# Kernel tuning notes

Measured on AMD Instinct MI355X. Metric: run time of the kernel, lower is better.

The kernel has to match this reference:

```python
import jax, jax.numpy as jnp
import numpy as np

EMBED_DIM = 1024
NUM_HEADS = 16
DEPTH = EMBED_DIM // NUM_HEADS  # 64
B, S = 4, 2048


def setup_inputs() -> dict:
    key = jax.random.key(0)
    ks = jax.random.split(key, 12)
    sc = 0.02
    return {
        "q": jax.random.normal(ks[0], (B, S, EMBED_DIM), jnp.float32),
        "k": jax.random.normal(ks[1], (B, S, EMBED_DIM), jnp.float32),
        "v": jax.random.normal(ks[2], (B, S, EMBED_DIM), jnp.float32),
        # per-head Dense(depth) weights stacked over heads: [H, D, depth]
        "wq": jax.random.normal(ks[3], (NUM_HEADS, EMBED_DIM, DEPTH), jnp.float32) * sc,
        "bq": jnp.zeros((NUM_HEADS, DEPTH), jnp.float32),
        "wk": jax.random.normal(ks[4], (NUM_HEADS, EMBED_DIM, DEPTH), jnp.float32) * sc,
        "bk": jnp.zeros((NUM_HEADS, DEPTH), jnp.float32),
        "wv": jax.random.normal(ks[5], (NUM_HEADS, EMBED_DIM, DEPTH), jnp.float32) * sc,
        "bv": jnp.zeros((NUM_HEADS, DEPTH), jnp.float32),
        # final Dense(embedding_dim): [D, D]
        "wo": jax.random.normal(ks[6], (EMBED_DIM, EMBED_DIM), jnp.float32) * sc,
        "bo": jnp.zeros((EMBED_DIM,), jnp.float32),
        "use_mask": 1,
    }


def reference(q, k, v, wq, bq, wk, bk, wv, bv, wo, bo, use_mask):
    # Batched per-head projections (equivalent to H separate Dense layers).
    qh = jnp.einsum('bsd,hde->bhse', q, wq) + bq[None, :, None, :]
    kh = jnp.einsum('bsd,hde->bhse', k, wk) + bk[None, :, None, :]
    vh = jnp.einsum('bsd,hde->bhse', v, wv) + bv[None, :, None, :]

    scale = 1.0 / jnp.sqrt(jnp.asarray(DEPTH, jnp.float32))
    logits = jnp.einsum('bhqe,bhke->bhqk', qh, kh) * scale  # [B,H,Sq,Sk]
    if use_mask:
        Sq, Sk = qh.shape[2], kh.shape[2]
        causal = jnp.triu(jnp.ones((Sq, Sk), jnp.float32), k=1)
        logits = logits + causal[None, None, :, :] * (-1e9)
    attn = jax.nn.softmax(logits, axis=-1)
    out_h = jnp.einsum('bhqk,bhke->bhqe', attn, vh)  # [B,H,Sq,depth]
    # concat heads along last dim -> [B,Sq,H*depth]
    bsz, H, Sq, dep = out_h.shape
    concat = out_h.transpose(0, 2, 1, 3).reshape(bsz, Sq, H * dep)
    return concat @ wo + bo
```

## Files before the change

### kernel.cpp

```cpp
#include <hip/hip_runtime.h>

#define B_ 4
#define S_ 2048
#define H_ 16
#define D_ 64
#define E_ 1024
#define M_ 8192

typedef __attribute__((ext_vector_type(8))) __bf16 bf16x8;
typedef __attribute__((ext_vector_type(4))) __bf16 bf16x4;
typedef __attribute__((ext_vector_type(4))) float f32x4;
typedef __attribute__((ext_vector_type(16))) float f32x16;

__device__ __forceinline__ void gload_lds16(const void* g, void* l) {
  __builtin_amdgcn_global_load_lds(
      (const __attribute__((address_space(1))) unsigned int*)g,
      (__attribute__((address_space(3))) unsigned int*)l, 16, 0, 0);
}

__device__ __forceinline__ unsigned pk2(float a, float b) {
  union { __bf16 h; unsigned short u; } ua, ub;
  ua.h = (__bf16)a; ub.h = (__bf16)b;
  return ((unsigned)ub.u << 16) | (unsigned)ua.u;
}

__global__ void cvt_all(const float* __restrict__ q, const float* __restrict__ k,
                        const float* __restrict__ v, __bf16* __restrict__ Aq,
                        __bf16* __restrict__ Ak, __bf16* __restrict__ Av) {
  const int y = blockIdx.y;
  const float* src = (y == 0) ? q : (y == 1) ? k : v;
  __bf16* dst = (y == 0) ? Aq : (y == 1) ? Ak : Av;
  const int i = blockIdx.x * blockDim.x + threadIdx.x;
  const float4 vv = ((const float4*)src)[i];
  bf16x4 o;
  o.x = (__bf16)vv.x; o.y = (__bf16)vv.y; o.z = (__bf16)vv.z; o.w = (__bf16)vv.w;
  ((bf16x4*)dst)[i] = o;
}

__global__ void pack_all(const float* __restrict__ wq, const float* __restrict__ wk,
                         const float* __restrict__ wv, const float* __restrict__ wo,
                         __bf16* __restrict__ Bq, __bf16* __restrict__ Bk,
                         __bf16* __restrict__ Bv, __bf16* __restrict__ Bo) {
  const int y = blockIdx.y;
  const int idx = blockIdx.x * 256 + threadIdx.x;
  const int n = idx >> 10, kk = idx & 1023;
  if (y < 3) {
    const float* w = (y == 0) ? wq : (y == 1) ? wk : wv;
    __bf16* out = (y == 0) ? Bq : (y == 1) ? Bk : Bv;
    out[idx] = (__bf16)w[((size_t)(n >> 6) << 16) + (kk << 6) + (n & 63)];
  } else {
    Bo[idx] = (__bf16)wo[((size_t)kk << 10) + n];
  }
}

template <int MODE>
__global__ __launch_bounds__(256) void gemm_bt(const __bf16* __restrict__ A,
                                               const __bf16* __restrict__ Bt,
                                               const float* __restrict__ bias,
                                               void* __restrict__ Cout) {
  constexpr int K = 1024;
  __shared__ __bf16 As[128 * 64];
  __shared__ __bf16 Bs[128 * 64];
  const int t = threadIdx.x;
  const int w = t >> 6, l = t & 63;
  const int m0 = blockIdx.x * 128, n0 = blockIdx.y * 128;
  f32x4 acc[4][4] = {};

  for (int kt = 0; kt < K / 64; ++kt) {
    const int kb = kt * 64;
#pragma unroll
    for (int j = 0; j < 4; ++j) {
      const int ci = (j * 4 + w) * 64 + l;
      const int row = ci >> 3;
      const int c = (ci & 7) ^ (row & 7);
      gload_lds16(A + (size_t)(m0 + row) * K + kb + c * 8, As + (j * 4 + w) * 512);
      gload_lds16(Bt + (size_t)(n0 + row) * K + kb + c * 8, Bs + (j * 4 + w) * 512);
    }
    __syncthreads();
#pragma unroll
    for (int kk = 0; kk < 64; kk += 32) {
      bf16x8 af[4], bfr[4];
#pragma unroll
      for (int f = 0; f < 4; ++f) {
        const int ra = (w >> 1) * 64 + f * 16 + (l & 15);
        const int ca = ((kk >> 3) + (l >> 4)) ^ (ra & 7);
        af[f] = *(const bf16x8*)(As + ra * 64 + ca * 8);
        const int rb = (w & 1) * 64 + f * 16 + (l & 15);
        const int cb = ((kk >> 3) + (l >> 4)) ^ (rb & 7);
        bfr[f] = *(const bf16x8*)(Bs + rb * 64 + cb * 8);
      }
#pragma unroll
      for (int mf = 0; mf < 4; ++mf)
#pragma unroll
        for (int nf = 0; nf < 4; ++nf)
          acc[mf][nf] = __builtin_amdgcn_mfma_f32_16x16x32_bf16(af[mf], bfr[nf],
                                                                acc[mf][nf], 0, 0, 0);
    }
    __syncthreads();
  }

#pragma unroll
  for (int mf = 0; mf < 4; ++mf) {
#pragma unroll
    for (int nf = 0; nf < 4; ++nf) {
#pragma unroll
      for (int r = 0; r < 4; ++r) {
        const int gm = m0 + (w >> 1) * 64 + mf * 16 + (l >> 4) * 4 + r;
        const int gn = n0 + (w & 1) * 64 + nf * 16 + (l & 15);
        const float val = acc[mf][nf][r] + ((MODE == 1) ? bias[gm] : bias[gn]);
        if constexpr (MODE == 0) {
          ((__bf16*)Cout)[(((size_t)(gm >> 11) * H_ + (gn >> 6)) * S_ + (gm & 2047)) * D_ + (gn & 63)] =
              (__bf16)val;
        } else if constexpr (MODE == 1) {
          ((__bf16*)Cout)[(((size_t)(gn >> 11) * H_ + (gm >> 6)) * D_ + (gm & 63)) * S_ + (gn & 2047)] =
              (__bf16)val;
        } else {
          ((float*)Cout)[(size_t)gm * 1024 + gn] = val;
        }
      }
    }
  }
}

__global__ __launch_bounds__(512, 2) void attn_fused(const __bf16* __restrict__ qh,
                                                     const __bf16* __restrict__ kh,
                                                     const __bf16* __restrict__ vT,
                                                     __bf16* __restrict__ concat,
                                                     const int* __restrict__ use_mask_p) {
  __shared__ __bf16 Ks[2][64 * 64];
  __shared__ __bf16 Vs[2][64 * 64];
  const int t = threadIdx.x, w = t >> 6, l = t & 63;
  const int lo = l & 31, hi = l >> 5;
  const int bh = blockIdx.x, pair = blockIdx.y;
  const int usemask = *use_mask_p;
  const __bf16* Qb = qh + (size_t)bh * S_ * D_;
  const __bf16* Kb = kh + (size_t)bh * S_ * D_;
  const __bf16* Vb = vT + (size_t)bh * D_ * S_;
  const int b = bh >> 4, hh = bh & 15;
  constexpr float CEXP = 0.125f * 1.4426950408889634f;

  const int srow = t >> 3;
  const int sc = (t & 7) ^ (srow & 7);

  int cur = 0;
  for (int half = 0; half < 2; ++half) {
    const int qt = half ? (7 - pair) : pair;
    const int qrow0 = qt * 256 + w * 32;
    const int nkt = usemask ? (4 * qt + 4) : (S_ / 64);
    const int ktw = usemask ? (4 * qt + (w >> 1)) : 100000;
    const int ktdiag = usemask ? (4 * qt + (w >> 1)) : -1;

    bf16x8 qf[4];
#pragma unroll
    for (int ks = 0; ks < 4; ++ks)
      qf[ks] = *(const bf16x8*)(Qb + (size_t)(qrow0 + lo) * D_ + ks * 16 + hi * 8);

    float m = -3e38f, ls = 0.f;
    f32x16 o0 = {}, o1 = {};

    gload_lds16(Kb + (size_t)(0 + srow) * D_ + sc * 8, &Ks[cur][w * 512]);
    gload_lds16(Vb + (size_t)srow * S_ + 0 + sc * 8, &Vs[cur][w * 512]);

    for (int kt = 0; kt < nkt; ++kt) {
      __builtin_amdgcn_sched_barrier(0);
      asm volatile("s_waitcnt vmcnt(0)" ::: "memory");
      __builtin_amdgcn_s_barrier();
      __builtin_amdgcn_sched_barrier(0);

      if (kt + 1 < nkt) {
        const int nxt = cur ^ 1;
        gload_lds16(Kb + (size_t)((kt + 1) * 64 + srow) * D_ + sc * 8, &Ks[nxt][w * 512]);
        gload_lds16(Vb + (size_t)srow * S_ + (kt + 1) * 64 + sc * 8, &Vs[nxt][w * 512]);
      }

      if (kt <= ktw) {
        f32x16 s0 = {}, s1 = {};
        __builtin_amdgcn_s_setprio(1);
#pragma unroll
        for (int ks = 0; ks < 4; ++ks) {
          const int ch = ((ks << 1) | hi) ^ (lo & 7);
          const bf16x8 k0 = *(const bf16x8*)(&Ks[cur][lo * 64 + ch * 8]);
          const bf16x8 k1 = *(const bf16x8*)(&Ks[cur][(32 + lo) * 64 + ch * 8]);
          s0 = __builtin_amdgcn_mfma_f32_32x32x16_bf16(k0, qf[ks], s0, 0, 0, 0);
          s1 = __builtin_amdgcn_mfma_f32_32x32x16_bf16(k1, qf[ks], s1, 0, 0, 0);
        }
        __builtin_amdgcn_s_setprio(0);

        if (kt == ktdiag) {
          const int qloc = ((w & 1) << 5) + lo;
#pragma unroll
          for (int r = 0; r < 16; ++r) {
            const int kv0 = (r & 3) + 8 * (r >> 2) + 4 * hi;
            if (kv0 > qloc) s0[r] = -1e30f;
            if (kv0 + 32 > qloc) s1[r] = -1e30f;
          }
        }

        float pm = s0[0];
#pragma unroll
        for (int r = 1; r < 16; ++r) pm = fmaxf(pm, s0[r]);
#pragma unroll
        for (int r = 0; r < 16; ++r) pm = fmaxf(pm, s1[r]);
        pm = fmaxf(pm, __shfl_xor(pm, 32));

        if (!__all(pm - m <= 64.0f)) {
          const float mn = fmaxf(m, pm);
          const float al = __builtin_amdgcn_exp2f((m - mn) * CEXP);
          m = mn;
          ls *= al;
          o0 *= al;
          o1 *= al;
        }

        unsigned W0[4][2], W1[4][2];
        float rs0 = 0.f, rs1 = 0.f;
#pragma unroll
        for (int j = 0; j < 4; ++j) {
          float p0 = __builtin_amdgcn_exp2f((s0[4 * j + 0] - m) * CEXP);
          float p1 = __builtin_amdgcn_exp2f((s0[4 * j + 1] - m) * CEXP);
          float p2 = __builtin_amdgcn_exp2f((s0[4 * j + 2] - m) * CEXP);
          float p3 = __builtin_amdgcn_exp2f((s0[4 * j + 3] - m) * CEXP);
          rs0 += (p0 + p1) + (p2 + p3);
          W0[j][0] = pk2(p0, p1);
          W0[j][1] = pk2(p2, p3);
          float q0 = __builtin_amdgcn_exp2f((s1[4 * j + 0] - m) * CEXP);
          float q1 = __builtin_amdgcn_exp2f((s1[4 * j + 1] - m) * CEXP);
          float q2 = __builtin_amdgcn_exp2f((s1[4 * j + 2] - m) * CEXP);
          float q3 = __builtin_amdgcn_exp2f((s1[4 * j + 3] - m) * CEXP);
          rs1 += (q0 + q1) + (q2 + q3);
          W1[j][0] = pk2(q0, q1);
          W1[j][1] = pk2(q2, q3);
        }
        float rs = rs0 + rs1;
        rs += __shfl_xor(rs, 32);
        ls += rs;

        bf16x8 pa[4];
#pragma unroll
        for (int ks = 0; ks < 4; ++ks) {
          const int c = ks & 1;
          unsigned x0, x1, y0, y1;
          if ((ks >> 1) == 0) {
            x0 = W0[2 * c][0]; x1 = W0[2 * c][1];
            y0 = W0[2 * c + 1][0]; y1 = W0[2 * c + 1][1];
          } else {
            x0 = W1[2 * c][0]; x1 = W1[2 * c][1];
            y0 = W1[2 * c + 1][0]; y1 = W1[2 * c + 1][1];
          }
          asm volatile("v_permlane32_swap_b32 %0, %1" : "+v"(x0), "+v"(y0));
          asm volatile("v_permlane32_swap_b32 %0, %1" : "+v"(x1), "+v"(y1));
          union { unsigned u[4]; bf16x8 v; } uu;
          uu.u[0] = x0; uu.u[1] = x1; uu.u[2] = y0; uu.u[3] = y1;
          pa[ks] = uu.v;
        }

        __builtin_amdgcn_s_setprio(1);
#pragma unroll
        for (int ks = 0; ks < 4; ++ks) {
          const int ch = ((ks << 1) | hi) ^ (lo & 7);
          const bf16x8 v0 = *(const bf16x8*)(&Vs[cur][lo * 64 + ch * 8]);
          const bf16x8 v1 = *(const bf16x8*)(&Vs[cur][(32 + lo) * 64 + ch * 8]);
          o0 = __builtin_amdgcn_mfma_f32_32x32x16_bf16(v0, pa[ks], o0, 0, 0, 0);
          o1 = __builtin_amdgcn_mfma_f32_32x32x16_bf16(v1, pa[ks], o1, 0, 0, 0);
        }
        __builtin_amdgcn_s_setprio(0);
      }
      cur ^= 1;
    }

    const float inv = 1.0f / ls;
    const size_t rowbase = ((size_t)(b * S_ + qrow0 + lo)) * E_ + hh * 64;
#pragma unroll
    for (int rr = 0; rr < 4; ++rr) {
      bf16x4 v0, v1;
#pragma unroll
      for (int bb = 0; bb < 4; ++bb) {
        v0[bb] = (__bf16)(o0[4 * rr + bb] * inv);
        v1[bb] = (__bf16)(o1[4 * rr + bb] * inv);
      }
      *(bf16x4*)(concat + rowbase + 8 * rr + 4 * hi) = v0;
      *(bf16x4*)(concat + rowbase + 32 + 8 * rr + 4 * hi) = v1;
    }
  }
}

extern "C" void kernel_launch(void* const* d_in, const int* in_sizes, int n_in,
                              void* d_out, int out_size, void* d_ws, size_t ws_size,
                              hipStream_t stream) {
  const float* q = (const float*)d_in[0];
  const float* k = (const float*)d_in[1];
  const float* v = (const float*)d_in[2];
  const float* wq = (const float*)d_in[3];
  const float* bq = (const float*)d_in[4];
  const float* wk = (const float*)d_in[5];
  const float* bk = (const float*)d_in[6];
  const float* wv = (const float*)d_in[7];
  const float* bv = (const float*)d_in[8];
  const float* wo = (const float*)d_in[9];
  const float* bo = (const float*)d_in[10];
  const int* use_mask = (const int*)d_in[11];
  (void)in_sizes; (void)n_in; (void)out_size; (void)ws_size;

  char* ws = (char*)d_ws;
  __bf16* Aq = (__bf16*)ws;
  __bf16* Ak = Aq + (size_t)M_ * E_;
  __bf16* Av = Ak + (size_t)M_ * E_;
  __bf16* Bq = Av + (size_t)M_ * E_;
  __bf16* Bk = Bq + (size_t)E_ * E_;
  __bf16* Bv = Bk + (size_t)E_ * E_;
  __bf16* Bo = Bv + (size_t)E_ * E_;
  __bf16* qhb = Bo + (size_t)E_ * E_;
  __bf16* khb = qhb + (size_t)8388608;
  __bf16* vTb = khb + (size_t)8388608;
  __bf16* concat = Aq;

  cvt_all<<<dim3(8192, 3), 256, 0, stream>>>(q, k, v, Aq, Ak, Av);
  pack_all<<<dim3(4096, 4), 256, 0, stream>>>(wq, wk, wv, wo, Bq, Bk, Bv, Bo);
  gemm_bt<0><<<dim3(64, 8), 256, 0, stream>>>(Aq, Bq, bq, qhb);
  gemm_bt<0><<<dim3(64, 8), 256, 0, stream>>>(Ak, Bk, bk, khb);
  gemm_bt<1><<<dim3(8, 64), 256, 0, stream>>>(Bv, Av, bv, vTb);
  attn_fused<<<dim3(64, 4), 512, 0, stream>>>(qhb, khb, vTb, concat, use_mask);
  gemm_bt<2><<<dim3(64, 8), 256, 0, stream>>>(concat, Bo, bo, d_out);
}
```

Measured before the change: 207.0 us.

## Give each attention wave 64 query rows and one q-tile per block

The attention kernel moves from 8 waves of 32 query rows to 4 waves of 64 query rows each, so every K/V fragment read from LDS feeds twice as many MFMAs. Each block now handles a single 256-row query tile, with 8 tiles in the y-grid ordered heaviest first, instead of pairing two tiles per block for load balance. The goal is less LDS read traffic per unit of work and more instruction-level parallelism per wave. The cost is higher register pressure from the doubled accumulators and Q fragments, and per-block work that is now uneven under the causal mask.

```diff
diff --git a/kernel.cpp b/kernel.cpp
--- a/kernel.cpp
+++ b/kernel.cpp
@@ -122,7 +122,7 @@
   }
 }
 
-__global__ __launch_bounds__(512, 2) void attn_fused(const __bf16* __restrict__ qh,
+__global__ __launch_bounds__(256, 2) void attn_fused(const __bf16* __restrict__ qh,
                                                      const __bf16* __restrict__ kh,
                                                      const __bf16* __restrict__ vT,
                                                      __bf16* __restrict__ concat,
@@ -131,7 +131,9 @@
   __shared__ __bf16 Vs[2][64 * 64];
   const int t = threadIdx.x, w = t >> 6, l = t & 63;
   const int lo = l & 31, hi = l >> 5;
-  const int bh = blockIdx.x, pair = blockIdx.y;
+  const int bh = blockIdx.x;
+  const int y = blockIdx.y;
+  const int qt = (y < 4) ? (7 - y) : (y - 4);
   const int usemask = *use_mask_p;
   const __bf16* Qb = qh + (size_t)bh * S_ * D_;
   const __bf16* Kb = kh + (size_t)bh * S_ * D_;
@@ -139,147 +141,196 @@
   const int b = bh >> 4, hh = bh & 15;
   constexpr float CEXP = 0.125f * 1.4426950408889634f;
 
-  const int srow = t >> 3;
-  const int sc = (t & 7) ^ (srow & 7);
+  const int qrow0 = qt * 256 + w * 64;
+  const int nkt = usemask ? (4 * qt + 4) : (S_ / 64);
+  const int ktw = usemask ? (4 * qt + w) : (1 << 30);
+
+  bf16x8 qfA[4], qfB[4];
+#pragma unroll
+  for (int ks = 0; ks < 4; ++ks) {
+    qfA[ks] = *(const bf16x8*)(Qb + (size_t)(qrow0 + lo) * D_ + ks * 16 + hi * 8);
+    qfB[ks] = *(const bf16x8*)(Qb + (size_t)(qrow0 + 32 + lo) * D_ + ks * 16 + hi * 8);
+  }
+
+  float mA = -3e38f, mB = -3e38f, lsA = 0.f, lsB = 0.f;
+  f32x16 oA0 = {}, oA1 = {}, oB0 = {}, oB1 = {};
 
   int cur = 0;
-  for (int half = 0; half < 2; ++half) {
-    const int qt = half ? (7 - pair) : pair;
-    const int qrow0 = qt * 256 + w * 32;
-    const int nkt = usemask ? (4 * qt + 4) : (S_ / 64);
-    const int ktw = usemask ? (4 * qt + (w >> 1)) : 100000;
-    const int ktdiag = usemask ? (4 * qt + (w >> 1)) : -1;
-
-    bf16x8 qf[4];
-#pragma unroll
-    for (int ks = 0; ks < 4; ++ks)
-      qf[ks] = *(const bf16x8*)(Qb + (size_t)(qrow0 + lo) * D_ + ks * 16 + hi * 8);
-
-    float m = -3e38f, ls = 0.f;
-    f32x16 o0 = {}, o1 = {};
-
-    gload_lds16(Kb + (size_t)(0 + srow) * D_ + sc * 8, &Ks[cur][w * 512]);
-    gload_lds16(Vb + (size_t)srow * S_ + 0 + sc * 8, &Vs[cur][w * 512]);
-
-    for (int kt = 0; kt < nkt; ++kt) {
-      __builtin_amdgcn_sched_barrier(0);
-      asm volatile("s_waitcnt vmcnt(0)" ::: "memory");
-      __builtin_amdgcn_s_barrier();
-      __builtin_amdgcn_sched_barrier(0);
-
-      if (kt + 1 < nkt) {
-        const int nxt = cur ^ 1;
-        gload_lds16(Kb + (size_t)((kt + 1) * 64 + srow) * D_ + sc * 8, &Ks[nxt][w * 512]);
-        gload_lds16(Vb + (size_t)srow * S_ + (kt + 1) * 64 + sc * 8, &Vs[nxt][w * 512]);
-      }
-
-      if (kt <= ktw) {
-        f32x16 s0 = {}, s1 = {};
-        __builtin_amdgcn_s_setprio(1);
-#pragma unroll
-        for (int ks = 0; ks < 4; ++ks) {
-          const int ch = ((ks << 1) | hi) ^ (lo & 7);
-          const bf16x8 k0 = *(const bf16x8*)(&Ks[cur][lo * 64 + ch * 8]);
-          const bf16x8 k1 = *(const bf16x8*)(&Ks[cur][(32 + lo) * 64 + ch * 8]);
-          s0 = __builtin_amdgcn_mfma_f32_32x32x16_bf16(k0, qf[ks], s0, 0, 0, 0);
-          s1 = __builtin_amdgcn_mfma_f32_32x32x16_bf16(k1, qf[ks], s1, 0, 0, 0);
-        }
-        __builtin_amdgcn_s_setprio(0);
-
-        if (kt == ktdiag) {
-          const int qloc = ((w & 1) << 5) + lo;
-#pragma unroll
-          for (int r = 0; r < 16; ++r) {
-            const int kv0 = (r & 3) + 8 * (r >> 2) + 4 * hi;
-            if (kv0 > qloc) s0[r] = -1e30f;
-            if (kv0 + 32 > qloc) s1[r] = -1e30f;
-          }
-        }
-
-        float pm = s0[0];
-#pragma unroll
-        for (int r = 1; r < 16; ++r) pm = fmaxf(pm, s0[r]);
-#pragma unroll
-        for (int r = 0; r < 16; ++r) pm = fmaxf(pm, s1[r]);
-        pm = fmaxf(pm, __shfl_xor(pm, 32));
-
-        if (!__all(pm - m <= 64.0f)) {
-          const float mn = fmaxf(m, pm);
-          const float al = __builtin_amdgcn_exp2f((m - mn) * CEXP);
-          m = mn;
-          ls *= al;
-          o0 *= al;
-          o1 *= al;
-        }
-
+  {
+#pragma unroll
+    for (int j = 0; j < 2; ++j) {
+      const int ci = j * 256 + t;
+      const int row = ci >> 3;
+      const int sc = (ci & 7) ^ (row & 7);
+      gload_lds16(Kb + (size_t)row * D_ + sc * 8, &Ks[0][j * 2048 + w * 512]);
+      gload_lds16(Vb + (size_t)row * S_ + sc * 8, &Vs[0][j * 2048 + w * 512]);
+    }
+  }
+
+  for (int kt = 0; kt < nkt; ++kt) {
+    __builtin_amdgcn_sched_barrier(0);
+    asm volatile("s_waitcnt vmcnt(0)" ::: "memory");
+    __builtin_amdgcn_s_barrier();
+    __builtin_amdgcn_sched_barrier(0);
+
+    if (kt + 1 < nkt) {
+      const int nxt = cur ^ 1;
+#pragma unroll
+      for (int j = 0; j < 2; ++j) {
+        const int ci = j * 256 + t;
+        const int row = ci >> 3;
+        const int sc = (ci & 7) ^ (row & 7);
+        gload_lds16(Kb + (size_t)((kt + 1) * 64 + row) * D_ + sc * 8,
+                    &Ks[nxt][j * 2048 + w * 512]);
+        gload_lds16(Vb + (size_t)row * S_ + (kt + 1) * 64 + sc * 8,
+                    &Vs[nxt][j * 2048 + w * 512]);
+      }
+    }
+
+    if (kt <= ktw) {
+      f32x16 sA0 = {}, sA1 = {}, sB0 = {}, sB1 = {};
+      __builtin_amdgcn_s_setprio(1);
+#pragma unroll
+      for (int ks = 0; ks < 4; ++ks) {
+        const int ch = ((ks << 1) | hi) ^ (lo & 7);
+        const bf16x8 k0 = *(const bf16x8*)(&Ks[cur][lo * 64 + ch * 8]);
+        const bf16x8 k1 = *(const bf16x8*)(&Ks[cur][(32 + lo) * 64 + ch * 8]);
+        sA0 = __builtin_amdgcn_mfma_f32_32x32x16_bf16(k0, qfA[ks], sA0, 0, 0, 0);
+        sA1 = __builtin_amdgcn_mfma_f32_32x32x16_bf16(k1, qfA[ks], sA1, 0, 0, 0);
+        sB0 = __builtin_amdgcn_mfma_f32_32x32x16_bf16(k0, qfB[ks], sB0, 0, 0, 0);
+        sB1 = __builtin_amdgcn_mfma_f32_32x32x16_bf16(k1, qfB[ks], sB1, 0, 0, 0);
+      }
+      __builtin_amdgcn_s_setprio(0);
+
+      if (usemask && kt == ktw) {
+#pragma unroll
+        for (int r = 0; r < 16; ++r) {
+          const int c = (r & 3) + 8 * (r >> 2) + 4 * hi;
+          if (c > lo) sA0[r] = -1e30f;
+          sA1[r] = -1e30f;
+          if (c > lo) sB1[r] = -1e30f;
+        }
+      }
+
+      float pmA = sA0[0], pmB = sB0[0];
+#pragma unroll
+      for (int r = 1; r < 16; ++r) { pmA = fmaxf(pmA, sA0[r]); pmB = fmaxf(pmB, sB0[r]); }
+#pragma unroll
+      for (int r = 0; r < 16; ++r) { pmA = fmaxf(pmA, sA1[r]); pmB = fmaxf(pmB, sB1[r]); }
+      pmA = fmaxf(pmA, __shfl_xor(pmA, 32));
+      pmB = fmaxf(pmB, __shfl_xor(pmB, 32));
+
+      if (!__all((pmA - mA <= 64.0f) && (pmB - mB <= 64.0f))) {
+        const float mnA = fmaxf(mA, pmA), mnB = fmaxf(mB, pmB);
+        const float alA = __builtin_amdgcn_exp2f((mA - mnA) * CEXP);
+        const float alB = __builtin_amdgcn_exp2f((mB - mnB) * CEXP);
+        mA = mnA; mB = mnB;
+        lsA *= alA; lsB *= alB;
+        oA0 *= alA; oA1 *= alA; oB0 *= alB; oB1 *= alB;
+      }
+
+      bf16x8 paA[4], paB[4];
+      {
         unsigned W0[4][2], W1[4][2];
-        float rs0 = 0.f, rs1 = 0.f;
+        float rs = 0.f;
 #pragma unroll
         for (int j = 0; j < 4; ++j) {
-          float p0 = __builtin_amdgcn_exp2f((s0[4 * j + 0] - m) * CEXP);
-          float p1 = __builtin_amdgcn_exp2f((s0[4 * j + 1] - m) * CEXP);
-          float p2 = __builtin_amdgcn_exp2f((s0[4 * j + 2] - m) * CEXP);
-          float p3 = __builtin_amdgcn_exp2f((s0[4 * j + 3] - m) * CEXP);
-          rs0 += (p0 + p1) + (p2 + p3);
-          W0[j][0] = pk2(p0, p1);
-          W0[j][1] = pk2(p2, p3);
-          float q0 = __builtin_amdgcn_exp2f((s1[4 * j + 0] - m) * CEXP);
-          float q1 = __builtin_amdgcn_exp2f((s1[4 * j + 1] - m) * CEXP);
-          float q2 = __builtin_amdgcn_exp2f((s1[4 * j + 2] - m) * CEXP);
-          float q3 = __builtin_amdgcn_exp2f((s1[4 * j + 3] - m) * CEXP);
-          rs1 += (q0 + q1) + (q2 + q3);
-          W1[j][0] = pk2(q0, q1);
-          W1[j][1] = pk2(q2, q3);
-        }
-        float rs = rs0 + rs1;
+          float p0 = __builtin_amdgcn_exp2f((sA0[4 * j + 0] - mA) * CEXP);
+          float p1 = __builtin_amdgcn_exp2f((sA0[4 * j + 1] - mA) * CEXP);
+          float p2 = __builtin_amdgcn_exp2f((sA0[4 * j + 2] - mA) * CEXP);
+          float p3 = __builtin_amdgcn_exp2f((sA0[4 * j + 3] - mA) * CEXP);
+          rs += (p0 + p1) + (p2 + p3);
+          W0[j][0] = pk2(p0, p1); W0[j][1] = pk2(p2, p3);
+          float q0 = __builtin_amdgcn_exp2f((sA1[4 * j + 0] - mA) * CEXP);
+          float q1 = __builtin_amdgcn_exp2f((sA1[4 * j + 1] - mA) * CEXP);
+          float q2 = __builtin_amdgcn_exp2f((sA1[4 * j + 2] - mA) * CEXP);
+          float q3 = __builtin_amdgcn_exp2f((sA1[4 * j + 3] - mA) * CEXP);
+          rs += (q0 + q1) + (q2 + q3);
+          W1[j][0] = pk2(q0, q1); W1[j][1] = pk2(q2, q3);
+        }
         rs += __shfl_xor(rs, 32);
-        ls += rs;
-
-        bf16x8 pa[4];
+        lsA += rs;
 #pragma unroll
         for (int ks = 0; ks < 4; ++ks) {
           const int c = ks & 1;
           unsigned x0, x1, y0, y1;
-          if ((ks >> 1) == 0) {
-            x0 = W0[2 * c][0]; x1 = W0[2 * c][1];
-            y0 = W0[2 * c + 1][0]; y1 = W0[2 * c + 1][1];
-          } else {
-            x0 = W1[2 * c][0]; x1 = W1[2 * c][1];
-            y0 = W1[2 * c + 1][0]; y1 = W1[2 * c + 1][1];
-          }
+          if ((ks >> 1) == 0) { x0 = W0[2 * c][0]; x1 = W0[2 * c][1]; y0 = W0[2 * c + 1][0]; y1 = W0[2 * c + 1][1]; }
+          else { x0 = W1[2 * c][0]; x1 = W1[2 * c][1]; y0 = W1[2 * c + 1][0]; y1 = W1[2 * c + 1][1]; }
           asm volatile("v_permlane32_swap_b32 %0, %1" : "+v"(x0), "+v"(y0));
           asm volatile("v_permlane32_swap_b32 %0, %1" : "+v"(x1), "+v"(y1));
           union { unsigned u[4]; bf16x8 v; } uu;
           uu.u[0] = x0; uu.u[1] = x1; uu.u[2] = y0; uu.u[3] = y1;
-          pa[ks] = uu.v;
-        }
-
-        __builtin_amdgcn_s_setprio(1);
+          paA[ks] = uu.v;
+        }
+      }
+      {
+        unsigned W0[4][2], W1[4][2];
+        float rs = 0.f;
+#pragma unroll
+        for (int j = 0; j < 4; ++j) {
+          float p0 = __builtin_amdgcn_exp2f((sB0[4 * j + 0] - mB) * CEXP);
+          float p1 = __builtin_amdgcn_exp2f((sB0[4 * j + 1] - mB) * CEXP);
+          float p2 = __builtin_amdgcn_exp2f((sB0[4 * j + 2] - mB) * CEXP);
+          float p3 = __builtin_amdgcn_exp2f((sB0[4 * j + 3] - mB) * CEXP);
+          rs += (p0 + p1) + (p2 + p3);
+          W0[j][0] = pk2(p0, p1); W0[j][1] = pk2(p2, p3);
+          float q0 = __builtin_amdgcn_exp2f((sB1[4 * j + 0] - mB) * CEXP);
+          float q1 = __builtin_amdgcn_exp2f((sB1[4 * j + 1] - mB) * CEXP);
+          float q2 = __builtin_amdgcn_exp2f((sB1[4 * j + 2] - mB) * CEXP);
+          float q3 = __builtin_amdgcn_exp2f((sB1[4 * j + 3] - mB) * CEXP);
+          rs += (q0 + q1) + (q2 + q3);
+          W1[j][0] = pk2(q0, q1); W1[j][1] = pk2(q2, q3);
+        }
+        rs += __shfl_xor(rs, 32);
+        lsB += rs;
 #pragma unroll
         for (int ks = 0; ks < 4; ++ks) {
-          const int ch = ((ks << 1) | hi) ^ (lo & 7);
-          const bf16x8 v0 = *(const bf16x8*)(&Vs[cur][lo * 64 + ch * 8]);
-          const bf16x8 v1 = *(const bf16x8*)(&Vs[cur][(32 + lo) * 64 + ch * 8]);
-          o0 = __builtin_amdgcn_mfma_f32_32x32x16_bf16(v0, pa[ks], o0, 0, 0, 0);
-          o1 = __builtin_amdgcn_mfma_f32_32x32x16_bf16(v1, pa[ks], o1, 0, 0, 0);
-        }
-        __builtin_amdgcn_s_setprio(0);
-      }
-      cur ^= 1;
-    }
-
-    const float inv = 1.0f / ls;
-    const size_t rowbase = ((size_t)(b * S_ + qrow0 + lo)) * E_ + hh * 64;
+          const int c = ks & 1;
+          unsigned x0, x1, y0, y1;
+          if ((ks >> 1) == 0) { x0 = W0[2 * c][0]; x1 = W0[2 * c][1]; y0 = W0[2 * c + 1][0]; y1 = W0[2 * c + 1][1]; }
+          else { x0 = W1[2 * c][0]; x1 = W1[2 * c][1]; y0 = W1[2 * c + 1][0]; y1 = W1[2 * c + 1][1]; }
+          asm volatile("v_permlane32_swap_b32 %0, %1" : "+v"(x0), "+v"(y0));
+          asm volatile("v_permlane32_swap_b32 %0, %1" : "+v"(x1), "+v"(y1));
+          union { unsigned u[4]; bf16x8 v; } uu;
+          uu.u[0] = x0; uu.u[1] = x1; uu.u[2] = y0; uu.u[3] = y1;
+          paB[ks] = uu.v;
+        }
+      }
+
+      __builtin_amdgcn_s_setprio(1);
+#pragma unroll
+      for (int ks = 0; ks < 4; ++ks) {
+        const int ch = ((ks << 1) | hi) ^ (lo & 7);
+        const bf16x8 v0 = *(const bf16x8*)(&Vs[cur][lo * 64 + ch * 8]);
+        const bf16x8 v1 = *(const bf16x8*)(&Vs[cur][(32 + lo) * 64 + ch * 8]);
+        oA0 = __builtin_amdgcn_mfma_f32_32x32x16_bf16(v0, paA[ks], oA0, 0, 0, 0);
+        oA1 = __builtin_amdgcn_mfma_f32_32x32x16_bf16(v1, paA[ks], oA1, 0, 0, 0);
+        oB0 = __builtin_amdgcn_mfma_f32_32x32x16_bf16(v0, paB[ks], oB0, 0, 0, 0);
+        oB1 = __builtin_amdgcn_mfma_f32_32x32x16_bf16(v1, paB[ks], oB1, 0, 0, 0);
+      }
+      __builtin_amdgcn_s_setprio(0);
+    }
+    cur ^= 1;
+  }
+
+  {
+    const float invA = 1.0f / lsA, invB = 1.0f / lsB;
+    const size_t rbA = ((size_t)(b * S_ + qrow0 + lo)) * E_ + hh * 64;
+    const size_t rbB = ((size_t)(b * S_ + qrow0 + 32 + lo)) * E_ + hh * 64;
 #pragma unroll
     for (int rr = 0; rr < 4; ++rr) {
-      bf16x4 v0, v1;
+      bf16x4 a0, a1, b0, b1;
 #pragma unroll
       for (int bb = 0; bb < 4; ++bb) {
-        v0[bb] = (__bf16)(o0[4 * rr + bb] * inv);
-        v1[bb] = (__bf16)(o1[4 * rr + bb] * inv);
-      }
-      *(bf16x4*)(concat + rowbase + 8 * rr + 4 * hi) = v0;
-      *(bf16x4*)(concat + rowbase + 32 + 8 * rr + 4 * hi) = v1;
+        a0[bb] = (__bf16)(oA0[4 * rr + bb] * invA);
+        a1[bb] = (__bf16)(oA1[4 * rr + bb] * invA);
+        b0[bb] = (__bf16)(oB0[4 * rr + bb] * invB);
+        b1[bb] = (__bf16)(oB1[4 * rr + bb] * invB);
+      }
+      *(bf16x4*)(concat + rbA + 8 * rr + 4 * hi) = a0;
+      *(bf16x4*)(concat + rbA + 32 + 8 * rr + 4 * hi) = a1;
+      *(bf16x4*)(concat + rbB + 8 * rr + 4 * hi) = b0;
+      *(bf16x4*)(concat + rbB + 32 + 8 * rr + 4 * hi) = b1;
     }
   }
 }
@@ -319,6 +370,6 @@
   gemm_bt<0><<<dim3(64, 8), 256, 0, stream>>>(Aq, Bq, bq, qhb);
   gemm_bt<0><<<dim3(64, 8), 256, 0, stream>>>(Ak, Bk, bk, khb);
   gemm_bt<1><<<dim3(8, 64), 256, 0, stream>>>(Bv, Av, bv, vTb);
-  attn_fused<<<dim3(64, 4), 512, 0, stream>>>(qhb, khb, vTb, concat, use_mask);
+  attn_fused<<<dim3(64, 8), 256, 0, stream>>>(qhb, khb, vTb, concat, use_mask);
   gemm_bt<2><<<dim3(64, 8), 256, 0, stream>>>(concat, Bo, bo, d_out);
 }
```

Result: no change. 210.5 us (+1.7%).

## Merge Q/K projection GEMMs and halve attention block size for more blocks

Applied to the files above, without the earlier changes.

Fuses the separate Q and K projection GEMM launches into one launch of 1024 blocks, so the GPU fills better and one launch is saved. The attention kernel moves from 512-thread blocks over 256-row query tiles to 256-thread blocks over 128-row tiles. That doubles the grid to 512 blocks, with K/V tile loads split across two passes per thread. The softmax exponent now uses one fma with a precomputed negative max instead of a subtract and a multiply. Smaller attention blocks share each K/V tile across fewer waves, which adds LDS and global traffic per unit of work.

```diff
diff --git a/kernel.cpp b/kernel.cpp
--- a/kernel.cpp
+++ b/kernel.cpp
@@ -53,6 +53,71 @@
   }
 }
 
+__global__ __launch_bounds__(256) void gemm_qk(
+    const __bf16* __restrict__ Aq, const __bf16* __restrict__ Ak,
+    const __bf16* __restrict__ Bq, const __bf16* __restrict__ Bk,
+    const float* __restrict__ bq, const float* __restrict__ bk,
+    __bf16* __restrict__ qhb, __bf16* __restrict__ khb) {
+  constexpr int K = 1024;
+  __shared__ __bf16 As[128 * 64];
+  __shared__ __bf16 Bs[128 * 64];
+  const int t = threadIdx.x;
+  const int w = t >> 6, l = t & 63;
+  const int isK = blockIdx.y >> 3;
+  const __bf16* A = isK ? Ak : Aq;
+  const __bf16* Bt = isK ? Bk : Bq;
+  const float* bias = isK ? bk : bq;
+  __bf16* C = isK ? khb : qhb;
+  const int m0 = blockIdx.x * 128, n0 = (blockIdx.y & 7) * 128;
+  f32x4 acc[4][4] = {};
+
+  for (int kt = 0; kt < K / 64; ++kt) {
+    const int kb = kt * 64;
+#pragma unroll
+    for (int j = 0; j < 4; ++j) {
+      const int ci = (j * 4 + w) * 64 + l;
+      const int row = ci >> 3;
+      const int c = (ci & 7) ^ (row & 7);
+      gload_lds16(A + (size_t)(m0 + row) * K + kb + c * 8, As + (j * 4 + w) * 512);
+      gload_lds16(Bt + (size_t)(n0 + row) * K + kb + c * 8, Bs + (j * 4 + w) * 512);
+    }
+    __syncthreads();
+#pragma unroll
+    for (int kk = 0; kk < 64; kk += 32) {
+      bf16x8 af[4], bfr[4];
+#pragma unroll
+      for (int f = 0; f < 4; ++f) {
+        const int ra = (w >> 1) * 64 + f * 16 + (l & 15);
+        const int ca = ((kk >> 3) + (l >> 4)) ^ (ra & 7);
+        af[f] = *(const bf16x8*)(As + ra * 64 + ca * 8);
+        const int rb = (w & 1) * 64 + f * 16 + (l & 15);
+        const int cb = ((kk >> 3) + (l >> 4)) ^ (rb & 7);
+        bfr[f] = *(const bf16x8*)(Bs + rb * 64 + cb * 8);
+      }
+#pragma unroll
+      for (int mf = 0; mf < 4; ++mf)
+#pragma unroll
+        for (int nf = 0; nf < 4; ++nf)
+          acc[mf][nf] = __builtin_amdgcn_mfma_f32_16x16x32_bf16(af[mf], bfr[nf],
+                                                                acc[mf][nf], 0, 0, 0);
+    }
+    __syncthreads();
+  }
+
+#pragma unroll
+  for (int mf = 0; mf < 4; ++mf)
+#pragma unroll
+    for (int nf = 0; nf < 4; ++nf)
+#pragma unroll
+      for (int r = 0; r < 4; ++r) {
+        const int gm = m0 + (w >> 1) * 64 + mf * 16 + (l >> 4) * 4 + r;
+        const int gn = n0 + (w & 1) * 64 + nf * 16 + (l & 15);
+        const float val = acc[mf][nf][r] + bias[gn];
+        C[(((size_t)(gm >> 11) * H_ + (gn >> 6)) * S_ + (gm & 2047)) * D_ + (gn & 63)] =
+            (__bf16)val;
+      }
+}
+
 template <int MODE>
 __global__ __launch_bounds__(256) void gemm_bt(const __bf16* __restrict__ A,
                                                const __bf16* __restrict__ Bt,
@@ -108,10 +173,7 @@
         const int gm = m0 + (w >> 1) * 64 + mf * 16 + (l >> 4) * 4 + r;
         const int gn = n0 + (w & 1) * 64 + nf * 16 + (l & 15);
         const float val = acc[mf][nf][r] + ((MODE == 1) ? bias[gm] : bias[gn]);
-        if constexpr (MODE == 0) {
-          ((__bf16*)Cout)[(((size_t)(gm >> 11) * H_ + (gn >> 6)) * S_ + (gm & 2047)) * D_ + (gn & 63)] =
-              (__bf16)val;
-        } else if constexpr (MODE == 1) {
+        if constexpr (MODE == 1) {
           ((__bf16*)Cout)[(((size_t)(gn >> 11) * H_ + (gm >> 6)) * D_ + (gm & 63)) * S_ + (gn & 2047)] =
               (__bf16)val;
         } else {
@@ -122,7 +184,7 @@
   }
 }
 
-__global__ __launch_bounds__(512, 2) void attn_fused(const __bf16* __restrict__ qh,
+__global__ __launch_bounds__(256, 2) void attn_fused(const __bf16* __restrict__ qh,
                                                      const __bf16* __restrict__ kh,
                                                      const __bf16* __restrict__ vT,
                                                      __bf16* __restrict__ concat,
@@ -131,7 +193,7 @@
   __shared__ __bf16 Vs[2][64 * 64];
   const int t = threadIdx.x, w = t >> 6, l = t & 63;
   const int lo = l & 31, hi = l >> 5;
-  const int bh = blockIdx.x, pair = blockIdx.y;
+  const int bh = blockIdx.x, pr = blockIdx.y;
   const int usemask = *use_mask_p;
   const __bf16* Qb = qh + (size_t)bh * S_ * D_;
   const __bf16* Kb = kh + (size_t)bh * S_ * D_;
@@ -139,16 +201,13 @@
   const int b = bh >> 4, hh = bh & 15;
   constexpr float CEXP = 0.125f * 1.4426950408889634f;
 
-  const int srow = t >> 3;
-  const int sc = (t & 7) ^ (srow & 7);
-
   int cur = 0;
   for (int half = 0; half < 2; ++half) {
-    const int qt = half ? (7 - pair) : pair;
-    const int qrow0 = qt * 256 + w * 32;
-    const int nkt = usemask ? (4 * qt + 4) : (S_ / 64);
-    const int ktw = usemask ? (4 * qt + (w >> 1)) : 100000;
-    const int ktdiag = usemask ? (4 * qt + (w >> 1)) : -1;
+    const int qt = half ? (15 - pr) : pr;
+    const int qrow0 = qt * 128 + w * 32;
+    const int nkt = usemask ? (2 * qt + 2) : (S_ / 64);
+    const int ktw = usemask ? (2 * qt + (w >> 1)) : 100000;
+    const int ktdiag = usemask ? (2 * qt + (w >> 1)) : -1;
 
     bf16x8 qf[4];
 #pragma unroll
@@ -158,8 +217,14 @@
     float m = -3e38f, ls = 0.f;
     f32x16 o0 = {}, o1 = {};
 
-    gload_lds16(Kb + (size_t)(0 + srow) * D_ + sc * 8, &Ks[cur][w * 512]);
-    gload_lds16(Vb + (size_t)srow * S_ + 0 + sc * 8, &Vs[cur][w * 512]);
+#pragma unroll
+    for (int j = 0; j < 2; ++j) {
+      const int ci = j * 256 + t;
+      const int row = ci >> 3;
+      const int sc = (ci & 7) ^ (row & 7);
+      gload_lds16(Kb + (size_t)row * D_ + sc * 8, &Ks[cur][j * 2048 + w * 512]);
+      gload_lds16(Vb + (size_t)row * S_ + sc * 8, &Vs[cur][j * 2048 + w * 512]);
+    }
 
     for (int kt = 0; kt < nkt; ++kt) {
       __builtin_amdgcn_sched_barrier(0);
@@ -169,8 +234,16 @@
 
       if (kt + 1 < nkt) {
         const int nxt = cur ^ 1;
-        gload_lds16(Kb + (size_t)((kt + 1) * 64 + srow) * D_ + sc * 8, &Ks[nxt][w * 512]);
-        gload_lds16(Vb + (size_t)srow * S_ + (kt + 1) * 64 + sc * 8, &Vs[nxt][w * 512]);
+#pragma unroll
+        for (int j = 0; j < 2; ++j) {
+          const int ci = j * 256 + t;
+          const int row = ci >> 3;
+          const int sc = (ci & 7) ^ (row & 7);
+          gload_lds16(Kb + (size_t)((kt + 1) * 64 + row) * D_ + sc * 8,
+                      &Ks[nxt][j * 2048 + w * 512]);
+          gload_lds16(Vb + (size_t)row * S_ + (kt + 1) * 64 + sc * 8,
+                      &Vs[nxt][j * 2048 + w * 512]);
+        }
       }
 
       if (kt <= ktw) {
@@ -211,22 +284,23 @@
           o0 *= al;
           o1 *= al;
         }
+        const float mneg = -m * CEXP;
 
         unsigned W0[4][2], W1[4][2];
         float rs0 = 0.f, rs1 = 0.f;
 #pragma unroll
         for (int j = 0; j < 4; ++j) {
-          float p0 = __builtin_amdgcn_exp2f((s0[4 * j + 0] - m) * CEXP);
-          float p1 = __builtin_amdgcn_exp2f((s0[4 * j + 1] - m) * CEXP);
-          float p2 = __builtin_amdgcn_exp2f((s0[4 * j + 2] - m) * CEXP);
-          float p3 = __builtin_amdgcn_exp2f((s0[4 * j + 3] - m) * CEXP);
+          float p0 = __builtin_amdgcn_exp2f(__builtin_fmaf(s0[4 * j + 0], CEXP, mneg));
+          float p1 = __builtin_amdgcn_exp2f(__builtin_fmaf(s0[4 * j + 1], CEXP, mneg));
+          float p2 = __builtin_amdgcn_exp2f(__builtin_fmaf(s0[4 * j + 2], CEXP, mneg));
+          float p3 = __builtin_amdgcn_exp2f(__builtin_fmaf(s0[4 * j + 3], CEXP, mneg));
           rs0 += (p0 + p1) + (p2 + p3);
           W0[j][0] = pk2(p0, p1);
           W0[j][1] = pk2(p2, p3);
-          float q0 = __builtin_amdgcn_exp2f((s1[4 * j + 0] - m) * CEXP);
-          float q1 = __builtin_amdgcn_exp2f((s1[4 * j + 1] - m) * CEXP);
-          float q2 = __builtin_amdgcn_exp2f((s1[4 * j + 2] - m) * CEXP);
-          float q3 = __builtin_amdgcn_exp2f((s1[4 * j + 3] - m) * CEXP);
+          float q0 = __builtin_amdgcn_exp2f(__builtin_fmaf(s1[4 * j + 0], CEXP, mneg));
+          float q1 = __builtin_amdgcn_exp2f(__builtin_fmaf(s1[4 * j + 1], CEXP, mneg));
+          float q2 = __builtin_amdgcn_exp2f(__builtin_fmaf(s1[4 * j + 2], CEXP, mneg));
+          float q3 = __builtin_amdgcn_exp2f(__builtin_fmaf(s1[4 * j + 3], CEXP, mneg));
           rs1 += (q0 + q1) + (q2 + q3);
           W1[j][0] = pk2(q0, q1);
           W1[j][1] = pk2(q2, q3);
@@ -316,9 +390,8 @@
 
   cvt_all<<<dim3(8192, 3), 256, 0, stream>>>(q, k, v, Aq, Ak, Av);
   pack_all<<<dim3(4096, 4), 256, 0, stream>>>(wq, wk, wv, wo, Bq, Bk, Bv, Bo);
-  gemm_bt<0><<<dim3(64, 8), 256, 0, stream>>>(Aq, Bq, bq, qhb);
-  gemm_bt<0><<<dim3(64, 8), 256, 0, stream>>>(Ak, Bk, bk, khb);
+  gemm_qk<<<dim3(64, 16), 256, 0, stream>>>(Aq, Ak, Bq, Bk, bq, bk, qhb, khb);
   gemm_bt<1><<<dim3(8, 64), 256, 0, stream>>>(Bv, Av, bv, vTb);
-  attn_fused<<<dim3(64, 4), 512, 0, stream>>>(qhb, khb, vTb, concat, use_mask);
+  attn_fused<<<dim3(64, 8), 256, 0, stream>>>(qhb, khb, vTb, concat, use_mask);
   gemm_bt<2><<<dim3(64, 8), 256, 0, stream>>>(concat, Bo, bo, d_out);
 }
```

New measurement: 197.9 us. 1.05x faster.
